# Kernel optimization log

Hardware: AMD Instinct MI355X
Metric: run time of the kernel (lower is better)

Reference implementation:

```python
import jax, jax.numpy as jnp
import numpy as np

IMAGE = 224
PAD = 30            # max_pad_size
CROP = IMAGE - 2 * PAD  # 164
NCAM = 3
B, T = 16, 16


def setup_inputs() -> dict:
    key = jax.random.key(0)
    ks = jax.random.split(key, 12)
    x = jax.random.normal(ks[0], (B, 3, T, IMAGE, IMAGE), dtype=jnp.float32)
    cam_idx = jax.random.randint(ks[1], (B,), 0, NCAM, dtype=jnp.int32)
    # original uses np.random.randint(1, max_pad+1)
    off_right = jax.random.randint(ks[2], (B,), 1, PAD + 1, dtype=jnp.int32)
    off_down = jax.random.randint(ks[3], (B,), 1, PAD + 1, dtype=jnp.int32)
    # learned pad strips, stacked over the 3 cam views (ParameterDict order)
    pad_up_1 = jax.random.normal(ks[4], (NCAM, 3, 1, IMAGE), dtype=jnp.float32)
    pad_up_10 = jax.random.normal(ks[5], (NCAM, 3, 10, IMAGE), dtype=jnp.float32)
    pad_down_1 = jax.random.normal(ks[6], (NCAM, 3, 1, IMAGE), dtype=jnp.float32)
    pad_down_10 = jax.random.normal(ks[7], (NCAM, 3, 10, IMAGE), dtype=jnp.float32)
    pad_left_1 = jax.random.normal(ks[8], (NCAM, 3, CROP, 1), dtype=jnp.float32)
    pad_left_10 = jax.random.normal(ks[9], (NCAM, 3, CROP, 10), dtype=jnp.float32)
    pad_right_1 = jax.random.normal(ks[10], (NCAM, 3, CROP, 1), dtype=jnp.float32)
    pad_right_10 = jax.random.normal(ks[11], (NCAM, 3, CROP, 10), dtype=jnp.float32)
    return dict(x=x, pad_up_1=pad_up_1, pad_up_10=pad_up_10,
                pad_down_1=pad_down_1, pad_down_10=pad_down_10,
                pad_left_1=pad_left_1, pad_left_10=pad_left_10,
                pad_right_1=pad_right_1, pad_right_10=pad_right_10,
                cam_idx=cam_idx, off_right=off_right, off_down=off_down)


def _build_prompt(ci, orr, od,
                  pad_up_1, pad_up_10, pad_down_1, pad_down_10,
                  pad_left_1, pad_left_10, pad_right_1, pad_right_10):
    # per-sample prompt image [3, IMAGE, IMAGE]; fused gather version of the
    # per-strip torch.cat construction.
    pu1 = pad_up_1[ci, :, 0, :]        # [3, W]
    pu10 = pad_up_10[ci]               # [3, 10, W]
    pd1 = pad_down_1[ci, :, 0, :]      # [3, W]
    pd10 = pad_down_10[ci]             # [3, 10, W]
    pl1 = pad_left_1[ci, :, :, 0]      # [3, CROP]
    pl10 = pad_left_10[ci]             # [3, CROP, 10]
    pr1 = pad_right_1[ci, :, :, 0]     # [3, CROP]
    pr10 = pad_right_10[ci]            # [3, CROP, 10]

    off_l = 2 * PAD - orr
    off_u = 2 * PAD - od
    n10_l, n1_l = off_l // 10, off_l % 10
    n10_u, n1_u = off_u // 10, off_u % 10
    n1_r = orr % 10
    n1_d = od % 10

    h = jnp.arange(IMAGE)
    w = jnp.arange(IMAGE)
    hh = h[:, None]                    # [H,1]
    ww = w[None, :]                    # [1,W]

    # top band: n10_u copies of 10-strip then n1_u copies of 1-strip
    up = jnp.where(hh < n10_u * 10, pu10[:, h % 10, :], pu1[:, None, :])  # [3,H,W]
    # bottom band: n1_d copies of 1-strip then 10-strips
    hd = hh - (IMAGE - od)
    di = jnp.mod(hd - n1_d, 10)[:, 0]
    down = jnp.where(hd < n1_d, pd1[:, None, :], pd10[:, di, :])          # [3,H,W]

    r = jnp.clip(h - off_u, 0, CROP - 1)                                   # [H]
    left = jnp.where(ww < n10_l * 10,
                     pl10[:, r[:, None], (w % 10)[None, :]],
                     pl1[:, r, None])                                      # [3,H,W]
    wd = w - (IMAGE - orr)
    ri = jnp.mod(wd - n1_r, 10)
    right = jnp.where(wd[None, :] < n1_r,
                      pr1[:, r, None],
                      pr10[:, r[:, None], ri[None, :]])                    # [3,H,W]

    mid = jnp.where(ww < off_l, left,
                    jnp.where(ww >= IMAGE - orr, right, jnp.float32(0.0)))
    return jnp.where(hh < off_u, up,
                     jnp.where(hh >= IMAGE - od, down, mid))               # [3,H,W]


def reference(x, pad_up_1, pad_up_10, pad_down_1, pad_down_10,
              pad_left_1, pad_left_10, pad_right_1, pad_right_10,
              cam_idx, off_right, off_down):
    build = lambda ci, orr, od: _build_prompt(
        ci, orr, od, pad_up_1, pad_up_10, pad_down_1, pad_down_10,
        pad_left_1, pad_left_10, pad_right_1, pad_right_10)
    prompt = jax.vmap(build)(cam_idx, off_right, off_down)  # [B,3,H,W]
    return x + prompt[:, :, None, :, :]                     # [B,3,T,H,W]
```

## Files before the change

### kernel.cpp

```cpp
#include <hip/hip_runtime.h>

#define IMAGE 224
#define PAD   30
#define CROP  164
#define BATCH 16
#define TT    16
#define W4    56

__global__ __launch_bounds__(256) void prompt_add_kernel(
    const float* __restrict__ x,
    const float* __restrict__ pu1,  const float* __restrict__ pu10,
    const float* __restrict__ pd1,  const float* __restrict__ pd10,
    const float* __restrict__ pl1,  const float* __restrict__ pl10,
    const float* __restrict__ pr1,  const float* __restrict__ pr10,
    const int* __restrict__ cam_idx,
    const int* __restrict__ off_right,
    const int* __restrict__ off_down,
    float* __restrict__ out)
{
    const int idx = blockIdx.x * blockDim.x + threadIdx.x;
    const int total = BATCH * 3 * TT * IMAGE * W4;
    if (idx >= total) return;

    const int w4 = idx % W4;
    const int h  = (idx / W4) % IMAGE;
    const int c  = (idx / (W4 * IMAGE * TT)) % 3;
    const int b  =  idx / (W4 * IMAGE * TT * 3);

    const int ci    = cam_idx[b];
    const int orr   = off_right[b];
    const int od    = off_down[b];
    const int off_l = 2 * PAD - orr;
    const int off_u = 2 * PAD - od;
    const int n10_l = off_l / 10;
    const int n10_u = off_u / 10;
    const int n1_r  = orr % 10;
    const int n1_d  = od % 10;

    const int w0      = w4 * 4;
    const int base_cc = ci * 3 + c;

    float p[4];

    if (h < off_u) {
        const float* rowp = (h < n10_u * 10)
            ? (pu10 + (size_t)(base_cc * 10 + (h % 10)) * IMAGE)
            : (pu1  + (size_t)base_cc * IMAGE);
        #pragma unroll
        for (int j = 0; j < 4; ++j) p[j] = rowp[w0 + j];
    } else if (h >= IMAGE - od) {
        const int hd = h - (IMAGE - od);
        const float* rowp = (hd < n1_d)
            ? (pd1  + (size_t)base_cc * IMAGE)
            : (pd10 + (size_t)(base_cc * 10 + ((hd - n1_d) % 10)) * IMAGE);
        #pragma unroll
        for (int j = 0; j < 4; ++j) p[j] = rowp[w0 + j];
    } else {
        int r = h - off_u;
        r = r < 0 ? 0 : (r > CROP - 1 ? CROP - 1 : r);
        #pragma unroll
        for (int j = 0; j < 4; ++j) {
            const int w = w0 + j;
            float v;
            if (w < off_l) {
                v = (w < n10_l * 10)
                    ? pl10[((size_t)base_cc * CROP + r) * 10 + (w % 10)]
                    : pl1 [ (size_t)base_cc * CROP + r];
            } else if (w >= IMAGE - orr) {
                const int wd = w - (IMAGE - orr);
                v = (wd < n1_r)
                    ? pr1 [ (size_t)base_cc * CROP + r]
                    : pr10[((size_t)base_cc * CROP + r) * 10 + ((wd - n1_r) % 10)];
            } else {
                v = 0.0f;
            }
            p[j] = v;
        }
    }

    const size_t off = (size_t)idx * 4;
    const float4 xv = *reinterpret_cast<const float4*>(x + off);
    float4 ov;
    ov.x = xv.x + p[0];
    ov.y = xv.y + p[1];
    ov.z = xv.z + p[2];
    ov.w = xv.w + p[3];
    *reinterpret_cast<float4*>(out + off) = ov;
}

extern "C" void kernel_launch(void* const* d_in, const int* in_sizes, int n_in,
                              void* d_out, int out_size, void* d_ws, size_t ws_size,
                              hipStream_t stream) {
    const float* x    = (const float*)d_in[0];
    const float* pu1  = (const float*)d_in[1];
    const float* pu10 = (const float*)d_in[2];
    const float* pd1  = (const float*)d_in[3];
    const float* pd10 = (const float*)d_in[4];
    const float* pl1  = (const float*)d_in[5];
    const float* pl10 = (const float*)d_in[6];
    const float* pr1  = (const float*)d_in[7];
    const float* pr10 = (const float*)d_in[8];
    const int* cam_idx   = (const int*)d_in[9];
    const int* off_right = (const int*)d_in[10];
    const int* off_down  = (const int*)d_in[11];
    float* out = (float*)d_out;

    const int total  = BATCH * 3 * TT * IMAGE * W4;
    const int block  = 256;
    const int grid   = (total + block - 1) / block;

    prompt_add_kernel<<<grid, block, 0, stream>>>(
        x, pu1, pu10, pd1, pd10, pl1, pl10, pr1, pr10,
        cam_idx, off_right, off_down, out);
}
```

Before: 275.6 us.

## Split into prompt-build kernel and streaming add kernel with nontemporal accesses

Builds the per-sample prompt image once into workspace (B*3*H*W), then runs a lean streaming kernel that adds it to x across T, with two float4 per thread and nontemporal loads and stores. The goal is to take the branchy gather logic out of the bandwidth-bound main pass and to avoid cache pollution. In exchange it adds a second launch and a small intermediate buffer that must be written and read back.

```diff
diff --git a/kernel.cpp b/kernel.cpp
--- a/kernel.cpp
+++ b/kernel.cpp
@@ -6,9 +6,12 @@
 #define BATCH 16
 #define TT    16
 #define W4    56
+#define PLANE4 (IMAGE * W4)
+#define PROMPT_F4 (BATCH * 3 * PLANE4)
 
-__global__ __launch_bounds__(256) void prompt_add_kernel(
-    const float* __restrict__ x,
+typedef float v4f __attribute__((ext_vector_type(4)));
+
+__global__ __launch_bounds__(256) void build_prompt_kernel(
     const float* __restrict__ pu1,  const float* __restrict__ pu10,
     const float* __restrict__ pd1,  const float* __restrict__ pd10,
     const float* __restrict__ pl1,  const float* __restrict__ pl10,
@@ -16,16 +19,15 @@
     const int* __restrict__ cam_idx,
     const int* __restrict__ off_right,
     const int* __restrict__ off_down,
-    float* __restrict__ out)
+    float* __restrict__ prompt)
 {
     const int idx = blockIdx.x * blockDim.x + threadIdx.x;
-    const int total = BATCH * 3 * TT * IMAGE * W4;
-    if (idx >= total) return;
+    if (idx >= PROMPT_F4) return;
 
     const int w4 = idx % W4;
     const int h  = (idx / W4) % IMAGE;
-    const int c  = (idx / (W4 * IMAGE * TT)) % 3;
-    const int b  =  idx / (W4 * IMAGE * TT * 3);
+    const int c  = (idx / PLANE4) % 3;
+    const int b  =  idx / (PLANE4 * 3);
 
     const int ci    = cam_idx[b];
     const int orr   = off_right[b];
@@ -78,14 +80,36 @@
         }
     }
 
-    const size_t off = (size_t)idx * 4;
-    const float4 xv = *reinterpret_cast<const float4*>(x + off);
-    float4 ov;
-    ov.x = xv.x + p[0];
-    ov.y = xv.y + p[1];
-    ov.z = xv.z + p[2];
-    ov.w = xv.w + p[3];
-    *reinterpret_cast<float4*>(out + off) = ov;
+    v4f pv = { p[0], p[1], p[2], p[3] };
+    *reinterpret_cast<v4f*>(prompt + (size_t)idx * 4) = pv;
+}
+
+__global__ __launch_bounds__(256) void add_prompt_kernel(
+    const float* __restrict__ x,
+    const float* __restrict__ prompt,
+    float* __restrict__ out)
+{
+    const int i0 = blockIdx.x * 512 + threadIdx.x;
+    const int i1 = i0 + 256;
+
+    const int bc0   = i0 / (PLANE4 * TT);
+    const int rem0  = i0 % PLANE4;
+    const int bc1   = i1 / (PLANE4 * TT);
+    const int rem1  = i1 % PLANE4;
+
+    const v4f xv0 = __builtin_nontemporal_load(
+        reinterpret_cast<const v4f*>(x + (size_t)i0 * 4));
+    const v4f xv1 = __builtin_nontemporal_load(
+        reinterpret_cast<const v4f*>(x + (size_t)i1 * 4));
+    const v4f pv0 = *reinterpret_cast<const v4f*>(
+        prompt + ((size_t)bc0 * PLANE4 + rem0) * 4);
+    const v4f pv1 = *reinterpret_cast<const v4f*>(
+        prompt + ((size_t)bc1 * PLANE4 + rem1) * 4);
+
+    __builtin_nontemporal_store(xv0 + pv0,
+        reinterpret_cast<v4f*>(out + (size_t)i0 * 4));
+    __builtin_nontemporal_store(xv1 + pv1,
+        reinterpret_cast<v4f*>(out + (size_t)i1 * 4));
 }
 
 extern "C" void kernel_launch(void* const* d_in, const int* in_sizes, int n_in,
@@ -103,13 +127,14 @@
     const int* cam_idx   = (const int*)d_in[9];
     const int* off_right = (const int*)d_in[10];
     const int* off_down  = (const int*)d_in[11];
-    float* out = (float*)d_out;
+    float* out    = (float*)d_out;
+    float* prompt = (float*)d_ws;
 
-    const int total  = BATCH * 3 * TT * IMAGE * W4;
-    const int block  = 256;
-    const int grid   = (total + block - 1) / block;
+    build_prompt_kernel<<<(PROMPT_F4 + 255) / 256, 256, 0, stream>>>(
+        pu1, pu10, pd1, pd10, pl1, pl10, pr1, pr10,
+        cam_idx, off_right, off_down, prompt);
 
-    prompt_add_kernel<<<grid, block, 0, stream>>>(
-        x, pu1, pu10, pd1, pd10, pl1, pl10, pr1, pr10,
-        cam_idx, off_right, off_down, out);
+    const int total_f4 = BATCH * 3 * TT * PLANE4;
+    const int grid2 = total_f4 / 512;
+    add_prompt_kernel<<<grid2, 256, 0, stream>>>(x, prompt, out);
 }
```

New measurement: 279.0 us. About the same (+1.2%).
